# Optimization experiments

Hardware: AMD Instinct MI355X
Metric: run time of the kernel (lower is better)

Reference implementation:

```python
import jax, jax.numpy as jnp
import numpy as np

N = 500_000          # nodes
E = 8_000_000        # edges (avg degree 16)
C = 2                # in/out channels
STEP_DIM = 8
NUM_STEPS = 100
K = 2                # k_hops -> powers [0, 1]
HID = 8              # hidden_layers


def setup_inputs() -> dict:
    key = jax.random.key(0)
    ks = jax.random.split(key, 6)
    X = jax.random.normal(ks[0], (N, C), dtype=jnp.float32)
    edge_index = jax.random.randint(ks[1], (2, E), 0, N, dtype=jnp.int32)
    step_emb = jax.random.normal(ks[2], (NUM_STEPS, STEP_DIM), dtype=jnp.float32)
    d_in0 = C + STEP_DIM  # 10
    # layer 0: one Linear per power p in {0,1}
    W0 = jax.random.normal(ks[3], (K, d_in0, C), dtype=jnp.float32) / np.sqrt(d_in0).astype(np.float32)
    b0 = jnp.zeros((K, C), dtype=jnp.float32)
    # layers 1..7, stacked for lax.scan
    Wh = jax.random.normal(ks[4], (HID - 1, K, C, C), dtype=jnp.float32) / np.sqrt(C).astype(np.float32)
    bh = jnp.zeros((HID - 1, K, C), dtype=jnp.float32)
    return dict(X=X, edge_index=edge_index, step_index=7, step_emb=step_emb,
                W0=W0, b0=b0, Wh=Wh, bh=bh)


def _make_prop(edge_index, n):
    """GCN-normalized propagation with self-loops (PyG gcn_norm), as used by MixHopConv."""
    src, dst = edge_index[0], edge_index[1]
    # in-degree on destination nodes, +1 for the self-loop
    deg = jnp.zeros((n,), jnp.float32).at[dst].add(1.0) + 1.0
    dis = jax.lax.rsqrt(deg)  # deg^{-1/2}; deg >= 1 so no inf handling needed
    edge_w = dis[src] * dis[dst]  # [E]

    def prop(x):
        msg = x[src] * edge_w[:, None]                      # [E, F] gather
        out = jax.ops.segment_sum(msg, dst, num_segments=n)  # [N, F] scatter-add
        return out + x * (dis * dis)[:, None]               # self-loop term
    return prop


def reference(X, edge_index, step_index, step_emb, W0, b0, Wh, bh):
    n = X.shape[0]
    prop = _make_prop(edge_index, n)

    s = jnp.broadcast_to(step_emb[step_index], (n, STEP_DIM))
    x = jnp.concatenate([X, s], axis=-1)  # [N, 10]

    # layer 0: concat(xW0, (Ax)W1) -> view(-1,K,C).sum(1) -> relu  ==  relu(xW0+b0 + (Ax)W1+b1)
    x = jax.nn.relu(x @ W0[0] + b0[0] + prop(x) @ W0[1] + b0[1])  # [N, 2]

    def body(x, wb):
        W, b = wb  # W: [K, C, C], b: [K, C]
        h = x @ W[0] + b[0] + prop(x) @ W[1] + b[1]
        return jax.nn.relu(h), None

    x, _ = jax.lax.scan(body, x, (Wh, bh))
    return x
```

## Files before the change

kernel.cpp:

```cpp
#include <hip/hip_runtime.h>


constexpr int NN = 500000;
constexpr int NE = 8000000;
constexpr int STEP_DIM = 8;
constexpr int HIDM1 = 7;

constexpr int BSH  = 10;
constexpr int BNOD = 1 << BSH;
constexpr int NBUK = (NN + BNOD - 1) / BNOD;
constexpr int NBLK = 250;
constexpr int EPB  = NE / NBLK;
constexpr int QPB  = EPB / 4;

constexpr int SLOT  = 18432;
constexpr int CPT   = SLOT / 512;
constexpr int WSPAN = 64 * CPT;
constexpr unsigned SENT = (unsigned)BNOD << 19;

__device__ __forceinline__ int swiz(int L) {
  int w = L / WSPAN;
  int r = L - w * WSPAN;
  int l = r / CPT;
  int o = r - l * CPT;
  return w * WSPAN + (o >> 2) * 256 + l * 4 + (o & 3);
}


__global__ __launch_bounds__(1024) void k_bhist(const int* __restrict__ dst,
                                                int* __restrict__ bhist) {
  __shared__ int hist[NBUK];
  int b = blockIdx.x, t = threadIdx.x;
  for (int h = t; h < NBUK; h += 1024) hist[h] = 0;
  __syncthreads();
  const int4* d4p = (const int4*)dst + (size_t)b * QPB;
  for (int i = t; i < QPB; i += 1024) {
    int4 d = d4p[i];
    atomicAdd(&hist[d.x >> BSH], 1);
    atomicAdd(&hist[d.y >> BSH], 1);
    atomicAdd(&hist[d.z >> BSH], 1);
    atomicAdd(&hist[d.w >> BSH], 1);
  }
  __syncthreads();
  for (int h = t; h < NBUK; h += 1024) bhist[h * NBLK + b] = hist[h];
}


__global__ __launch_bounds__(256) void k_rowscan(int* __restrict__ bhist,
                                                 int* __restrict__ bcount) {
  __shared__ int sm[256];
  int h = blockIdx.x, t = threadIdx.x;
  int v = (t < NBLK) ? bhist[h * NBLK + t] : 0;
  sm[t] = v;
  __syncthreads();
  for (int o = 1; o < 256; o <<= 1) {
    int x = (t >= o) ? sm[t - o] : 0;
    __syncthreads();
    sm[t] += x;
    __syncthreads();
  }
  if (t < NBLK) bhist[h * NBLK + t] = sm[t] - v;
  if (t == 255) bcount[h] = sm[255];
}


__global__ __launch_bounds__(1024) void k_bscatter(const int* __restrict__ src,
                                                   const int* __restrict__ dst,
                                                   const int* __restrict__ off,
                                                   unsigned int* __restrict__ col2) {
  __shared__ int cur[NBUK];
  int b = blockIdx.x, t = threadIdx.x;
  for (int h = t; h < NBUK; h += 1024) cur[h] = h * SLOT + off[h * NBLK + b];
  __syncthreads();
  const int4* s4p = (const int4*)src + (size_t)b * QPB;
  const int4* d4p = (const int4*)dst + (size_t)b * QPB;
  for (int i = t; i < QPB; i += 1024) {
    int4 s = s4p[i];
    int4 d = d4p[i];
    int p0 = atomicAdd(&cur[d.x >> BSH], 1);
    col2[p0] = ((unsigned)(d.x & (BNOD - 1)) << 19) | (unsigned)s.x;
    int p1 = atomicAdd(&cur[d.y >> BSH], 1);
    col2[p1] = ((unsigned)(d.y & (BNOD - 1)) << 19) | (unsigned)s.y;
    int p2 = atomicAdd(&cur[d.z >> BSH], 1);
    col2[p2] = ((unsigned)(d.z & (BNOD - 1)) << 19) | (unsigned)s.z;
    int p3 = atomicAdd(&cur[d.w >> BSH], 1);
    col2[p3] = ((unsigned)(d.w & (BNOD - 1)) << 19) | (unsigned)s.w;
  }
}


__global__ __launch_bounds__(512) void k_sort(unsigned int* __restrict__ col2,
                                              const int* __restrict__ bcount,
                                              const float2* __restrict__ X,
                                              float* __restrict__ dis,
                                              float2* __restrict__ xs0) {
  __shared__ unsigned stage[SLOT];
  __shared__ int hist[BNOD];
  __shared__ int tsum[512];
  int b = blockIdx.x, t = threadIdx.x;
  int ns = bcount[b];
  if (ns > SLOT) ns = SLOT;
  unsigned* base = col2 + (size_t)b * SLOT;
  hist[2 * t] = 0;
  hist[2 * t + 1] = 0;
  __syncthreads();
  for (int i = t; i < ns; i += 512) {
    unsigned p = base[i];
    stage[i] = p;
    atomicAdd(&hist[p >> 19], 1);
  }
  __syncthreads();
  int a0 = hist[2 * t], a1 = hist[2 * t + 1];
  tsum[t] = a0 + a1;
  __syncthreads();
  for (int o = 1; o < 512; o <<= 1) {
    int v = (t >= o) ? tsum[t - o] : 0;
    __syncthreads();
    tsum[t] += v;
    __syncthreads();
  }
  int ex = tsum[t] - (a0 + a1);
  hist[2 * t] = ex;
  hist[2 * t + 1] = ex + a0;
  __syncthreads();
  for (int i = t; i < ns; i += 512) {
    unsigned p = stage[i];
    int pos = atomicAdd(&hist[p >> 19], 1);
    base[swiz(pos)] = p;
  }
  for (int L = ns + t; L < SLOT; L += 512) base[swiz(L)] = SENT;
  int nb = b << BSH;
  int i0 = nb + 2 * t;
  if (i0 < NN) {
    float d = rsqrtf((float)a0 + 1.0f);
    dis[i0] = d;
    float2 x = X[i0];
    xs0[i0] = make_float2(d * x.x, d * x.y);
  }
  int i1 = i0 + 1;
  if (i1 < NN) {
    float d = rsqrtf((float)a1 + 1.0f);
    dis[i1] = d;
    float2 x = X[i1];
    xs0[i1] = make_float2(d * x.x, d * x.y);
  }
}


__global__ __launch_bounds__(512) void k_sd(const unsigned int* __restrict__ col2,
                                            const float* __restrict__ dis,
                                            float* __restrict__ sd) {
  __shared__ float acc[BNOD + 1];
  int b = blockIdx.x, t = threadIdx.x;
  for (int j = t; j < BNOD + 1; j += 512) acc[j] = 0.f;
  __syncthreads();
  const unsigned* base = col2 + (size_t)b * SLOT + (t >> 6) * WSPAN;
  int l4 = (t & 63) * 4;
  int cur = BNOD;
  float r = 0.f;
#pragma unroll
  for (int i = 0; i < CPT / 4; ++i) {
    int4 q = *(const int4*)(base + i * 256 + l4);
#pragma unroll
    for (int j = 0; j < 4; ++j) {
      unsigned p = ((const unsigned*)&q)[j];
      float v = dis[p & 0x7FFFF];
      int ld = (int)(p >> 19);
      if (ld != cur) {
        atomicAdd(&acc[cur], r);
        cur = ld;
        r = v;
      } else {
        r += v;
      }
    }
  }
  atomicAdd(&acc[cur], r);
  __syncthreads();
  int nb = b << BSH;
#pragma unroll
  for (int j = 0; j < 2; ++j) {
    int l = t + j * 512;
    int i = nb + l;
    if (i < NN) sd[i] = acc[l];
  }
}

__global__ __launch_bounds__(512) void k_blayer0(const unsigned int* __restrict__ col2,
                                                 const float2* __restrict__ xs0,
                                                 const float2* __restrict__ X,
                                                 const float* __restrict__ dis,
                                                 const float* __restrict__ sd,
                                                 const float* __restrict__ W0,
                                                 const float* __restrict__ b0,
                                                 const float* __restrict__ step_emb,
                                                 const int* __restrict__ step_index,
                                                 float2* __restrict__ xs_out) {
  __shared__ float acc[(BNOD + 1) * 2];
  int b = blockIdx.x, t = threadIdx.x;
  for (int j = t; j < (BNOD + 1) * 2; j += 512) acc[j] = 0.f;
  __syncthreads();
  const unsigned* base = col2 + (size_t)b * SLOT + (t >> 6) * WSPAN;
  int l4 = (t & 63) * 4;
  int cur = BNOD;
  float rx = 0.f, ry = 0.f;
#pragma unroll
  for (int i = 0; i < CPT / 4; ++i) {
    int4 q = *(const int4*)(base + i * 256 + l4);
#pragma unroll
    for (int j = 0; j < 4; ++j) {
      unsigned p = ((const unsigned*)&q)[j];
      float2 v = xs0[p & 0x7FFFF];
      int ld = (int)(p >> 19);
      if (ld != cur) {
        atomicAdd(&acc[cur * 2 + 0], rx);
        atomicAdd(&acc[cur * 2 + 1], ry);
        cur = ld;
        rx = v.x;
        ry = v.y;
      } else {
        rx += v.x;
        ry += v.y;
      }
    }
  }
  atomicAdd(&acc[cur * 2 + 0], rx);
  atomicAdd(&acc[cur * 2 + 1], ry);
  __syncthreads();
  const float* sv = step_emb + step_index[0] * STEP_DIM;
  float c0[2], c1[2];
#pragma unroll
  for (int o = 0; o < 2; ++o) {
    float a0 = b0[o] + b0[2 + o];
    float a1 = 0.f;
#pragma unroll
    for (int j = 0; j < STEP_DIM; ++j) {
      a0 += sv[j] * W0[(2 + j) * 2 + o];
      a1 += sv[j] * W0[20 + (2 + j) * 2 + o];
    }
    c0[o] = a0;
    c1[o] = a1;
  }
  int nb = b << BSH;
#pragma unroll
  for (int j = 0; j < 2; ++j) {
    int l = t + j * 512;
    int i = nb + l;
    if (i < NN) {
      float d = dis[i], d2 = d * d;
      float2 x = X[i];
      float px = d * acc[l * 2 + 0] + d2 * x.x;
      float py = d * acc[l * 2 + 1] + d2 * x.y;
      float rowsum = d * sd[i] + d2;
      float h0 = c0[0] + rowsum * c1[0] + x.x * W0[0] + x.y * W0[2] + px * W0[20] + py * W0[22];
      float h1 = c0[1] + rowsum * c1[1] + x.x * W0[1] + x.y * W0[3] + px * W0[21] + py * W0[23];
      h0 = fmaxf(h0, 0.f);
      h1 = fmaxf(h1, 0.f);
      xs_out[i] = make_float2(d * h0, d * h1);
    }
  }
}

__global__ __launch_bounds__(512) void k_blayer(const unsigned int* __restrict__ col2,
                                                const float* __restrict__ dis,
                                                const float2* __restrict__ xs_in,
                                                const float* __restrict__ W,
                                                const float* __restrict__ bb,
                                                float2* __restrict__ xs_out,
                                                float2* __restrict__ out,
                                                int last) {
  __shared__ float acc[(BNOD + 1) * 2];
  int b = blockIdx.x, t = threadIdx.x;
  for (int j = t; j < (BNOD + 1) * 2; j += 512) acc[j] = 0.f;
  __syncthreads();
  const unsigned* base = col2 + (size_t)b * SLOT + (t >> 6) * WSPAN;
  int l4 = (t & 63) * 4;
  int cur = BNOD;
  float rx = 0.f, ry = 0.f;
#pragma unroll
  for (int i = 0; i < CPT / 4; ++i) {
    int4 q = *(const int4*)(base + i * 256 + l4);
#pragma unroll
    for (int j = 0; j < 4; ++j) {
      unsigned p = ((const unsigned*)&q)[j];
      float2 v = xs_in[p & 0x7FFFF];
      int ld = (int)(p >> 19);
      if (ld != cur) {
        atomicAdd(&acc[cur * 2 + 0], rx);
        atomicAdd(&acc[cur * 2 + 1], ry);
        cur = ld;
        rx = v.x;
        ry = v.y;
      } else {
        rx += v.x;
        ry += v.y;
      }
    }
  }
  atomicAdd(&acc[cur * 2 + 0], rx);
  atomicAdd(&acc[cur * 2 + 1], ry);
  __syncthreads();
  int nb = b << BSH;
#pragma unroll
  for (int j = 0; j < 2; ++j) {
    int l = t + j * 512;
    int i = nb + l;
    if (i < NN) {
      float d = dis[i];
      float2 xsv = xs_in[i];
      float inv = 1.0f / d;
      float xx = xsv.x * inv, xy = xsv.y * inv;
      float px = d * (acc[l * 2 + 0] + xsv.x);
      float py = d * (acc[l * 2 + 1] + xsv.y);
      float h0 = bb[0] + bb[2] + xx * W[0] + xy * W[2] + px * W[4] + py * W[6];
      float h1 = bb[1] + bb[3] + xx * W[1] + xy * W[3] + px * W[5] + py * W[7];
      h0 = fmaxf(h0, 0.f);
      h1 = fmaxf(h1, 0.f);
      if (last) {
        out[i] = make_float2(h0, h1);
      } else {
        xs_out[i] = make_float2(d * h0, d * h1);
      }
    }
  }
}


extern "C" void kernel_launch(void* const* d_in, const int* in_sizes, int n_in,
                              void* d_out, int out_size, void* d_ws, size_t ws_size,
                              hipStream_t stream) {
  const float2* X        = (const float2*)d_in[0];
  const int*    edge     = (const int*)d_in[1];
  const int*    src      = edge;
  const int*    dstp     = edge + NE;
  const int*    step_idx = (const int*)d_in[2];
  const float*  step_emb = (const float*)d_in[3];
  const float*  W0       = (const float*)d_in[4];
  const float*  b0       = (const float*)d_in[5];
  const float*  Wh       = (const float*)d_in[6];
  const float*  bbias    = (const float*)d_in[7];

  int*      ip     = (int*)d_ws;
  unsigned* col2   = (unsigned*)ip;
  size_t    o      = (size_t)NBUK * SLOT;
  int*      bhist  = ip + o;            o += (size_t)NBUK * NBLK + 6;
  int*      bcount = ip + o;            o += 512;
  float*    dis    = (float*)(ip + o);  o += 500224;
  float*    sd     = (float*)(ip + o);  o += 500224;
  float2*   bufA   = (float2*)(ip + o); o += 2 * 500224;
  float2*   bufB   = (float2*)(ip + o);

  k_bhist<<<NBLK, 1024, 0, stream>>>(dstp, bhist);
  k_rowscan<<<NBUK, 256, 0, stream>>>(bhist, bcount);
  k_bscatter<<<NBLK, 1024, 0, stream>>>(src, dstp, bhist, col2);
  k_sort<<<NBUK, 512, 0, stream>>>(col2, bcount, X, dis, bufA);
  k_sd<<<NBUK, 512, 0, stream>>>(col2, dis, sd);

  k_blayer0<<<NBUK, 512, 0, stream>>>(col2, bufA, X, dis, sd, W0, b0,
                                      step_emb, step_idx, bufB);
  float2* cur = bufB;
  float2* nxt = bufA;
  for (int l = 0; l < HIDM1; ++l) {
    k_blayer<<<NBUK, 512, 0, stream>>>(col2, dis, cur, Wh + l * 8,
                                       bbias + l * 4, nxt, (float2*)d_out,
                                       l == HIDM1 - 1 ? 1 : 0);
    float2* tmp = cur;
    cur = nxt;
    nxt = tmp;
  }
}
```

Before: 638.0 us.

## Halve bucket size, fuse degree-sum pass into layer 0, prefetch edge chunk

Buckets shrink from 1024 to 512 nodes, so each 512-thread block handles one node per thread, and the bucket slot, scatter block count and swizzle layout change to match. The separate k_sd pass, which summed neighbour dis values, is removed. That sum is now accumulated as a third channel inside k_blayer0's gather. Each thread loads its 18 packed edges up front with nontemporal vector loads (four 16-byte and one 8-byte) before the gather loop, aiming to raise memory-level parallelism and cut one full pass over the edge list. The trade-offs are twice as many buckets with SLOT=9216, which leaves less headroom for bucket overflow, and more LDS atomics in layer 0.

```diff
diff --git a/kernel.cpp b/kernel.cpp
--- a/kernel.cpp
+++ b/kernel.cpp
@@ -6,24 +6,29 @@
 constexpr int STEP_DIM = 8;
 constexpr int HIDM1 = 7;
 
-constexpr int BSH  = 10;
+constexpr int BSH  = 9;
 constexpr int BNOD = 1 << BSH;
 constexpr int NBUK = (NN + BNOD - 1) / BNOD;
-constexpr int NBLK = 250;
+constexpr int NBLK = 125;
 constexpr int EPB  = NE / NBLK;
 constexpr int QPB  = EPB / 4;
 
-constexpr int SLOT  = 18432;
+constexpr int SLOT  = 9216;
 constexpr int CPT   = SLOT / 512;
 constexpr int WSPAN = 64 * CPT;
 constexpr unsigned SENT = (unsigned)BNOD << 19;
+
+typedef unsigned u32x4 __attribute__((ext_vector_type(4)));
+typedef unsigned u32x2 __attribute__((ext_vector_type(2)));
 
 __device__ __forceinline__ int swiz(int L) {
   int w = L / WSPAN;
   int r = L - w * WSPAN;
   int l = r / CPT;
   int o = r - l * CPT;
-  return w * WSPAN + (o >> 2) * 256 + l * 4 + (o & 3);
+  int base = w * WSPAN;
+  return (o < 16) ? base + (o >> 2) * 256 + l * 4 + (o & 3)
+                  : base + 1024 + l * 2 + (o - 16);
 }
 
 
@@ -46,21 +51,21 @@
 }
 
 
-__global__ __launch_bounds__(256) void k_rowscan(int* __restrict__ bhist,
+__global__ __launch_bounds__(128) void k_rowscan(int* __restrict__ bhist,
                                                  int* __restrict__ bcount) {
-  __shared__ int sm[256];
+  __shared__ int sm[128];
   int h = blockIdx.x, t = threadIdx.x;
   int v = (t < NBLK) ? bhist[h * NBLK + t] : 0;
   sm[t] = v;
   __syncthreads();
-  for (int o = 1; o < 256; o <<= 1) {
+  for (int o = 1; o < 128; o <<= 1) {
     int x = (t >= o) ? sm[t - o] : 0;
     __syncthreads();
     sm[t] += x;
     __syncthreads();
   }
   if (t < NBLK) bhist[h * NBLK + t] = sm[t] - v;
-  if (t == 255) bcount[h] = sm[255];
+  if (t == 127) bcount[h] = sm[127];
 }
 
 
@@ -101,8 +106,7 @@
   int ns = bcount[b];
   if (ns > SLOT) ns = SLOT;
   unsigned* base = col2 + (size_t)b * SLOT;
-  hist[2 * t] = 0;
-  hist[2 * t + 1] = 0;
+  hist[t] = 0;
   __syncthreads();
   for (int i = t; i < ns; i += 512) {
     unsigned p = base[i];
@@ -110,8 +114,8 @@
     atomicAdd(&hist[p >> 19], 1);
   }
   __syncthreads();
-  int a0 = hist[2 * t], a1 = hist[2 * t + 1];
-  tsum[t] = a0 + a1;
+  int a = hist[t];
+  tsum[t] = a;
   __syncthreads();
   for (int o = 1; o < 512; o <<= 1) {
     int v = (t >= o) ? tsum[t - o] : 0;
@@ -119,9 +123,7 @@
     tsum[t] += v;
     __syncthreads();
   }
-  int ex = tsum[t] - (a0 + a1);
-  hist[2 * t] = ex;
-  hist[2 * t + 1] = ex + a0;
+  hist[t] = tsum[t] - a;
   __syncthreads();
   for (int i = t; i < ns; i += 512) {
     unsigned p = stage[i];
@@ -129,103 +131,65 @@
     base[swiz(pos)] = p;
   }
   for (int L = ns + t; L < SLOT; L += 512) base[swiz(L)] = SENT;
-  int nb = b << BSH;
-  int i0 = nb + 2 * t;
-  if (i0 < NN) {
-    float d = rsqrtf((float)a0 + 1.0f);
-    dis[i0] = d;
-    float2 x = X[i0];
-    xs0[i0] = make_float2(d * x.x, d * x.y);
-  }
-  int i1 = i0 + 1;
-  if (i1 < NN) {
-    float d = rsqrtf((float)a1 + 1.0f);
-    dis[i1] = d;
-    float2 x = X[i1];
-    xs0[i1] = make_float2(d * x.x, d * x.y);
-  }
-}
-
-
-__global__ __launch_bounds__(512) void k_sd(const unsigned int* __restrict__ col2,
-                                            const float* __restrict__ dis,
-                                            float* __restrict__ sd) {
-  __shared__ float acc[BNOD + 1];
-  int b = blockIdx.x, t = threadIdx.x;
-  for (int j = t; j < BNOD + 1; j += 512) acc[j] = 0.f;
-  __syncthreads();
-  const unsigned* base = col2 + (size_t)b * SLOT + (t >> 6) * WSPAN;
-  int l4 = (t & 63) * 4;
-  int cur = BNOD;
-  float r = 0.f;
-#pragma unroll
-  for (int i = 0; i < CPT / 4; ++i) {
-    int4 q = *(const int4*)(base + i * 256 + l4);
-#pragma unroll
-    for (int j = 0; j < 4; ++j) {
-      unsigned p = ((const unsigned*)&q)[j];
-      float v = dis[p & 0x7FFFF];
-      int ld = (int)(p >> 19);
-      if (ld != cur) {
-        atomicAdd(&acc[cur], r);
-        cur = ld;
-        r = v;
-      } else {
-        r += v;
-      }
-    }
-  }
-  atomicAdd(&acc[cur], r);
-  __syncthreads();
-  int nb = b << BSH;
-#pragma unroll
-  for (int j = 0; j < 2; ++j) {
-    int l = t + j * 512;
-    int i = nb + l;
-    if (i < NN) sd[i] = acc[l];
-  }
-}
+  int i = (b << BSH) + t;
+  if (i < NN) {
+    float d = rsqrtf((float)a + 1.0f);
+    dis[i] = d;
+    float2 x = X[i];
+    xs0[i] = make_float2(d * x.x, d * x.y);
+  }
+}
+
 
 __global__ __launch_bounds__(512) void k_blayer0(const unsigned int* __restrict__ col2,
                                                  const float2* __restrict__ xs0,
                                                  const float2* __restrict__ X,
                                                  const float* __restrict__ dis,
-                                                 const float* __restrict__ sd,
                                                  const float* __restrict__ W0,
                                                  const float* __restrict__ b0,
                                                  const float* __restrict__ step_emb,
                                                  const int* __restrict__ step_index,
                                                  float2* __restrict__ xs_out) {
-  __shared__ float acc[(BNOD + 1) * 2];
-  int b = blockIdx.x, t = threadIdx.x;
-  for (int j = t; j < (BNOD + 1) * 2; j += 512) acc[j] = 0.f;
-  __syncthreads();
-  const unsigned* base = col2 + (size_t)b * SLOT + (t >> 6) * WSPAN;
-  int l4 = (t & 63) * 4;
+  __shared__ float acc[(BNOD + 1) * 3];
+  int b = blockIdx.x, t = threadIdx.x;
+  for (int j = t; j < (BNOD + 1) * 3; j += 512) acc[j] = 0.f;
+  __syncthreads();
+  const unsigned* bp = col2 + (size_t)b * SLOT + (t >> 6) * WSPAN;
+  int l = t & 63;
   int cur = BNOD;
-  float rx = 0.f, ry = 0.f;
-#pragma unroll
-  for (int i = 0; i < CPT / 4; ++i) {
-    int4 q = *(const int4*)(base + i * 256 + l4);
-#pragma unroll
-    for (int j = 0; j < 4; ++j) {
-      unsigned p = ((const unsigned*)&q)[j];
-      float2 v = xs0[p & 0x7FFFF];
-      int ld = (int)(p >> 19);
-      if (ld != cur) {
-        atomicAdd(&acc[cur * 2 + 0], rx);
-        atomicAdd(&acc[cur * 2 + 1], ry);
-        cur = ld;
-        rx = v.x;
-        ry = v.y;
-      } else {
-        rx += v.x;
-        ry += v.y;
-      }
+  float rx = 0.f, ry = 0.f, rd = 0.f;
+  unsigned ebuf[CPT];
+#pragma unroll
+  for (int i = 0; i < 4; ++i) {
+    u32x4 q = __builtin_nontemporal_load((const u32x4*)(bp + i * 256 + l * 4));
+#pragma unroll
+    for (int j = 0; j < 4; ++j) ebuf[i * 4 + j] = q[j];
+  }
+  {
+    u32x2 q2 = __builtin_nontemporal_load((const u32x2*)(bp + 1024 + l * 2));
+    ebuf[16] = q2[0];
+    ebuf[17] = q2[1];
+  }
+#pragma unroll
+  for (int o = 0; o < CPT; ++o) {
+    unsigned p = ebuf[o];
+    int s = p & 0x7FFFF;
+    float2 v = xs0[s];
+    float dv = dis[s];
+    int ld = (int)(p >> 19);
+    if (ld != cur) {
+      atomicAdd(&acc[cur * 3 + 0], rx);
+      atomicAdd(&acc[cur * 3 + 1], ry);
+      atomicAdd(&acc[cur * 3 + 2], rd);
+      cur = ld;
+      rx = v.x; ry = v.y; rd = dv;
+    } else {
+      rx += v.x; ry += v.y; rd += dv;
     }
   }
-  atomicAdd(&acc[cur * 2 + 0], rx);
-  atomicAdd(&acc[cur * 2 + 1], ry);
+  atomicAdd(&acc[cur * 3 + 0], rx);
+  atomicAdd(&acc[cur * 3 + 1], ry);
+  atomicAdd(&acc[cur * 3 + 2], rd);
   __syncthreads();
   const float* sv = step_emb + step_index[0] * STEP_DIM;
   float c0[2], c1[2];
@@ -241,23 +205,18 @@
     c0[o] = a0;
     c1[o] = a1;
   }
-  int nb = b << BSH;
-#pragma unroll
-  for (int j = 0; j < 2; ++j) {
-    int l = t + j * 512;
-    int i = nb + l;
-    if (i < NN) {
-      float d = dis[i], d2 = d * d;
-      float2 x = X[i];
-      float px = d * acc[l * 2 + 0] + d2 * x.x;
-      float py = d * acc[l * 2 + 1] + d2 * x.y;
-      float rowsum = d * sd[i] + d2;
-      float h0 = c0[0] + rowsum * c1[0] + x.x * W0[0] + x.y * W0[2] + px * W0[20] + py * W0[22];
-      float h1 = c0[1] + rowsum * c1[1] + x.x * W0[1] + x.y * W0[3] + px * W0[21] + py * W0[23];
-      h0 = fmaxf(h0, 0.f);
-      h1 = fmaxf(h1, 0.f);
-      xs_out[i] = make_float2(d * h0, d * h1);
-    }
+  int i = (b << BSH) + t;
+  if (i < NN) {
+    float d = dis[i], d2 = d * d;
+    float2 x = X[i];
+    float px = d * acc[t * 3 + 0] + d2 * x.x;
+    float py = d * acc[t * 3 + 1] + d2 * x.y;
+    float rowsum = d * acc[t * 3 + 2] + d2;
+    float h0 = c0[0] + rowsum * c1[0] + x.x * W0[0] + x.y * W0[2] + px * W0[20] + py * W0[22];
+    float h1 = c0[1] + rowsum * c1[1] + x.x * W0[1] + x.y * W0[3] + px * W0[21] + py * W0[23];
+    h0 = fmaxf(h0, 0.f);
+    h1 = fmaxf(h1, 0.f);
+    xs_out[i] = make_float2(d * h0, d * h1);
   }
 }
 
@@ -273,54 +232,55 @@
   int b = blockIdx.x, t = threadIdx.x;
   for (int j = t; j < (BNOD + 1) * 2; j += 512) acc[j] = 0.f;
   __syncthreads();
-  const unsigned* base = col2 + (size_t)b * SLOT + (t >> 6) * WSPAN;
-  int l4 = (t & 63) * 4;
+  const unsigned* bp = col2 + (size_t)b * SLOT + (t >> 6) * WSPAN;
+  int l = t & 63;
   int cur = BNOD;
   float rx = 0.f, ry = 0.f;
-#pragma unroll
-  for (int i = 0; i < CPT / 4; ++i) {
-    int4 q = *(const int4*)(base + i * 256 + l4);
-#pragma unroll
-    for (int j = 0; j < 4; ++j) {
-      unsigned p = ((const unsigned*)&q)[j];
-      float2 v = xs_in[p & 0x7FFFF];
-      int ld = (int)(p >> 19);
-      if (ld != cur) {
-        atomicAdd(&acc[cur * 2 + 0], rx);
-        atomicAdd(&acc[cur * 2 + 1], ry);
-        cur = ld;
-        rx = v.x;
-        ry = v.y;
-      } else {
-        rx += v.x;
-        ry += v.y;
-      }
+  unsigned ebuf[CPT];
+#pragma unroll
+  for (int i = 0; i < 4; ++i) {
+    u32x4 q = __builtin_nontemporal_load((const u32x4*)(bp + i * 256 + l * 4));
+#pragma unroll
+    for (int j = 0; j < 4; ++j) ebuf[i * 4 + j] = q[j];
+  }
+  {
+    u32x2 q2 = __builtin_nontemporal_load((const u32x2*)(bp + 1024 + l * 2));
+    ebuf[16] = q2[0];
+    ebuf[17] = q2[1];
+  }
+#pragma unroll
+  for (int o = 0; o < CPT; ++o) {
+    unsigned p = ebuf[o];
+    float2 v = xs_in[p & 0x7FFFF];
+    int ld = (int)(p >> 19);
+    if (ld != cur) {
+      atomicAdd(&acc[cur * 2 + 0], rx);
+      atomicAdd(&acc[cur * 2 + 1], ry);
+      cur = ld;
+      rx = v.x; ry = v.y;
+    } else {
+      rx += v.x; ry += v.y;
     }
   }
   atomicAdd(&acc[cur * 2 + 0], rx);
   atomicAdd(&acc[cur * 2 + 1], ry);
   __syncthreads();
-  int nb = b << BSH;
-#pragma unroll
-  for (int j = 0; j < 2; ++j) {
-    int l = t + j * 512;
-    int i = nb + l;
-    if (i < NN) {
-      float d = dis[i];
-      float2 xsv = xs_in[i];
-      float inv = 1.0f / d;
-      float xx = xsv.x * inv, xy = xsv.y * inv;
-      float px = d * (acc[l * 2 + 0] + xsv.x);
-      float py = d * (acc[l * 2 + 1] + xsv.y);
-      float h0 = bb[0] + bb[2] + xx * W[0] + xy * W[2] + px * W[4] + py * W[6];
-      float h1 = bb[1] + bb[3] + xx * W[1] + xy * W[3] + px * W[5] + py * W[7];
-      h0 = fmaxf(h0, 0.f);
-      h1 = fmaxf(h1, 0.f);
-      if (last) {
-        out[i] = make_float2(h0, h1);
-      } else {
-        xs_out[i] = make_float2(d * h0, d * h1);
-      }
+  int i = (b << BSH) + t;
+  if (i < NN) {
+    float d = dis[i];
+    float2 xsv = xs_in[i];
+    float inv = 1.0f / d;
+    float xx = xsv.x * inv, xy = xsv.y * inv;
+    float px = d * (acc[t * 2 + 0] + xsv.x);
+    float py = d * (acc[t * 2 + 1] + xsv.y);
+    float h0 = bb[0] + bb[2] + xx * W[0] + xy * W[2] + px * W[4] + py * W[6];
+    float h1 = bb[1] + bb[3] + xx * W[1] + xy * W[3] + px * W[5] + py * W[7];
+    h0 = fmaxf(h0, 0.f);
+    h1 = fmaxf(h1, 0.f);
+    if (last) {
+      out[i] = make_float2(h0, h1);
+    } else {
+      xs_out[i] = make_float2(d * h0, d * h1);
     }
   }
 }
@@ -343,20 +303,18 @@
   int*      ip     = (int*)d_ws;
   unsigned* col2   = (unsigned*)ip;
   size_t    o      = (size_t)NBUK * SLOT;
-  int*      bhist  = ip + o;            o += (size_t)NBUK * NBLK + 6;
-  int*      bcount = ip + o;            o += 512;
+  int*      bhist  = ip + o;            o += 122128;
+  int*      bcount = ip + o;            o += 1024;
   float*    dis    = (float*)(ip + o);  o += 500224;
-  float*    sd     = (float*)(ip + o);  o += 500224;
   float2*   bufA   = (float2*)(ip + o); o += 2 * 500224;
   float2*   bufB   = (float2*)(ip + o);
 
   k_bhist<<<NBLK, 1024, 0, stream>>>(dstp, bhist);
-  k_rowscan<<<NBUK, 256, 0, stream>>>(bhist, bcount);
+  k_rowscan<<<NBUK, 128, 0, stream>>>(bhist, bcount);
   k_bscatter<<<NBLK, 1024, 0, stream>>>(src, dstp, bhist, col2);
   k_sort<<<NBUK, 512, 0, stream>>>(col2, bcount, X, dis, bufA);
-  k_sd<<<NBUK, 512, 0, stream>>>(col2, dis, sd);
-
-  k_blayer0<<<NBUK, 512, 0, stream>>>(col2, bufA, X, dis, sd, W0, b0,
+
+  k_blayer0<<<NBUK, 512, 0, stream>>>(col2, bufA, X, dis, W0, b0,
                                       step_emb, step_idx, bufB);
   float2* cur = bufB;
   float2* nxt = bufA;
```

Result: slower. 679.0 us (+6.4%).
